# Performance work log

Hardware: AMD Instinct MI355X
Metric: run time of the kernel (lower is better)

Reference implementation:

```python
import jax, jax.numpy as jnp
import numpy as np

N, D_IN, D_OUT = 8192, 1024, 1024

def setup_inputs() -> dict:
    key = jax.random.key(0)
    k1, k2, k3, k4 = jax.random.split(key, 4)
    scale = 1.0 / np.sqrt(D_IN).astype(np.float32)
    return {
        "X": jax.random.normal(k1, (N, D_IN), dtype=jnp.float32),
        "W_Q": jax.random.normal(k2, (D_IN, D_OUT), dtype=jnp.float32) * scale,
        "W_K": jax.random.normal(k3, (D_IN, D_OUT), dtype=jnp.float32) * scale,
        "W_V": jax.random.normal(k4, (D_IN, D_OUT), dtype=jnp.float32) * scale,
    }

def reference(X, W_Q, W_K, W_V):
    # Manual single-head self-attention over the N rows of X.
    Q = X @ W_Q            # [N, d_out]
    Kmat = X @ W_K         # [N, d_out]
    V = X @ W_V            # [N, d_out]
    inv_sqrt_d = jnp.asarray(1.0 / np.sqrt(W_Q.shape[1]), dtype=Q.dtype)
    scores = (Q @ Kmat.T) * inv_sqrt_d            # [N, N]
    attn = jax.nn.softmax(scores, axis=-1)        # row-wise softmax (Keras default axis=-1)
    return attn @ V                               # [N, d_out]
```

## Files before the change

kernel.cpp:

```cpp
#include <hip/hip_runtime.h>

#define N_ROWS 8192
#define D_DIM  1024
#define SM_SHIFT 4.0f

typedef _Float16 f16;
typedef _Float16 f16x8 __attribute__((ext_vector_type(8)));
typedef _Float16 f16x4 __attribute__((ext_vector_type(4)));
typedef float    f32x4 __attribute__((ext_vector_type(4)));

__device__ __forceinline__ void gload16(const void* g, void* l) {
  __builtin_amdgcn_global_load_lds(
      (const __attribute__((address_space(1))) void*)g,
      (__attribute__((address_space(3))) void*)l, 16, 0, 0);
}

__device__ __forceinline__ int xcd_swz(int bid, int nb) {
  return (bid & 7) * (nb >> 3) + (bid >> 3);
}

__device__ __forceinline__ void tile2d4(int bid, int ny_t, int& nx, int& ny) {
  const int v = xcd_swz(bid, 32 * ny_t);
  const int g = v >> 4, w = v & 15;
  const int gpc = ny_t >> 2;
  const int gx = g / gpc, gy = g - gx * gpc;
  nx = gx * 4 + (w & 3);
  ny = gy * 4 + (w >> 2);
}

__global__ __launch_bounds__(256) void f32_to_f16_kernel(
    const float* __restrict__ in, f16* __restrict__ out, int n4) {
  for (int i = blockIdx.x * blockDim.x + threadIdx.x; i < n4;
       i += gridDim.x * blockDim.x) {
    float4 x = ((const float4*)in)[i];
    f16x4 h = {(f16)x.x, (f16)x.y, (f16)x.z, (f16)x.w};
    ((f16x4*)out)[i] = h;
  }
}

__global__ __launch_bounds__(256) void transpose_w_kernel(
    const float* __restrict__ w0, const float* __restrict__ w1,
    const float* __restrict__ w2, f16* __restrict__ WT) {
  const float* W = (blockIdx.z == 0) ? w0 : (blockIdx.z == 1) ? w1 : w2;
  f16* T = WT + (size_t)blockIdx.z * D_DIM * D_DIM;
  __shared__ float tile[64][65];
  const int r0 = blockIdx.y * 64, c0 = blockIdx.x * 64;
  const int t = threadIdx.x;
#pragma unroll
  for (int rep = 0; rep < 16; ++rep) {
    int idx = rep * 256 + t;
    int r = idx >> 6, c = idx & 63;
    tile[r][c] = W[(size_t)(r0 + r) * D_DIM + (c0 + c)];
  }
  __syncthreads();
#pragma unroll
  for (int rep = 0; rep < 16; ++rep) {
    int idx = rep * 256 + t;
    int r = idx >> 6, c = idx & 63;
    T[(size_t)(c0 + r) * D_DIM + (r0 + c)] = (f16)tile[c][r];
  }
}

template <bool SWAP>
__device__ __forceinline__ void mainloop256(const f16* __restrict__ Ag, int lda,
                                            const f16* __restrict__ Bg,
                                            int ldbt, int nk, f16* LA, f16* LB,
                                            f32x4 (&acc)[8][4], int tid) {
  const int lane = tid & 63;
  const int wr = tid >> 8, wc = (tid >> 6) & 3;
  const int ro = lane & 15;
  const int jj0 = (((lane >> 4) ^ (ro & 7)) << 4);
  const int rs = tid >> 3;
  const int ce = ((tid & 7) ^ (rs & 7)) * 8;
  const f16* a[4];
  const f16* b[4];
#pragma unroll
  for (int s = 0; s < 4; ++s) {
    a[s] = Ag + (size_t)(rs + 64 * s) * lda + ce;
    b[s] = Bg + (size_t)(rs + 64 * s) * ldbt + ce;
  }
  char* la = (char*)LA;
  char* lb = (char*)LB;
  const int t16 = tid * 16;

  auto stage_p0 = [&](int buf) {
    char* A = la + buf * 32768;
    char* B = lb + buf * 32768;
    gload16(a[0], A + t16);
    gload16(a[2], A + 16384 + t16);
    gload16(b[0], B + t16);
    gload16(b[1], B + 8192 + t16);
  };
  auto stage_p1 = [&](int buf) {
    char* A = la + buf * 32768;
    char* B = lb + buf * 32768;
    gload16(b[2], B + 16384 + t16);
    gload16(b[3], B + 24576 + t16);
    gload16(a[1], A + 8192 + t16);
    gload16(a[3], A + 24576 + t16);
#pragma unroll
    for (int s = 0; s < 4; ++s) {
      a[s] += 64;
      b[s] += 64;
    }
  };

  f16x8 af[4], bf[4];
  auto readA = [&](const char* ab, int h, int jo) {
#pragma unroll
    for (int j = 0; j < 4; ++j)
      af[j] = *(const f16x8*)(ab + (wr * 128 + h * 64 + j * 16 + ro) * 128 + jo);
  };
  auto readB = [&](const char* bb, int jo) {
#pragma unroll
    for (int ni = 0; ni < 4; ++ni)
      bf[ni] = *(const f16x8*)(bb + (wc * 64 + ni * 16 + ro) * 128 + jo);
  };

#define MFMA_CLUSTER(H)                                                   \
  asm volatile("s_waitcnt lgkmcnt(0)" ::: "memory");                      \
  __builtin_amdgcn_sched_barrier(0);                                      \
  __builtin_amdgcn_s_setprio(1);                                          \
  _Pragma("unroll") for (int j = 0; j < 4; ++j)                           \
  _Pragma("unroll") for (int ni = 0; ni < 4; ++ni)                        \
      acc[(H) * 4 + j][ni] =                                              \
          SWAP ? __builtin_amdgcn_mfma_f32_16x16x32_f16(bf[ni], af[j],    \
                                                        acc[(H) * 4 + j][ni], \
                                                        0, 0, 0)          \
               : __builtin_amdgcn_mfma_f32_16x16x32_f16(af[j], bf[ni],    \
                                                        acc[(H) * 4 + j][ni], \
                                                        0, 0, 0);         \
  __builtin_amdgcn_s_setprio(0);

  stage_p0(0);
  stage_p1(0);
  asm volatile("s_waitcnt vmcnt(0)" ::: "memory");
  __builtin_amdgcn_s_barrier();
  __builtin_amdgcn_sched_barrier(0);

  for (int kt = 0; kt < nk; ++kt) {
    const int buf = kt & 1;
    const char* ab = la + buf * 32768;
    const char* bb = lb + buf * 32768;
    const bool more = (kt + 1 < nk);
    readA(ab, 0, jj0);
    readB(bb, jj0);
    if (more) {
      stage_p0(buf ^ 1);
      asm volatile("s_waitcnt vmcnt(4)" ::: "memory");
    } else {
      asm volatile("s_waitcnt vmcnt(0)" ::: "memory");
    }
    __builtin_amdgcn_s_barrier();
    __builtin_amdgcn_sched_barrier(0);
    MFMA_CLUSTER(0)
    readA(ab, 1, jj0);
    if (more) stage_p1(buf ^ 1);
    MFMA_CLUSTER(1)
    readA(ab, 0, jj0 ^ 64);
    readB(bb, jj0 ^ 64);
    MFMA_CLUSTER(0)
    readA(ab, 1, jj0 ^ 64);
    MFMA_CLUSTER(1)
    asm volatile("s_waitcnt vmcnt(2)" ::: "memory");
    __builtin_amdgcn_s_barrier();
    __builtin_amdgcn_sched_barrier(0);
  }
#undef MFMA_CLUSTER
}

#define ACC_INIT8(acc)                                \
  _Pragma("unroll") for (int i = 0; i < 8; ++i)       \
      _Pragma("unroll") for (int j = 0; j < 4; ++j)   \
          acc[i][j] = (f32x4){0.f, 0.f, 0.f, 0.f};

__global__ __launch_bounds__(512, 2) void gemm_qkv(
    const f16* __restrict__ Xh, const f16* __restrict__ WT,
    f16* __restrict__ Q, f16* __restrict__ Kh, f16* __restrict__ VT) {
  __shared__ f16 LA[2][16384], LB[2][16384];
  const int v = xcd_swz(blockIdx.x, 384);
  const int z = v >> 7, r = v & 127;
  const int nx = r & 3, ny = r >> 2;
  const int tid = threadIdx.x, lane = tid & 63;
  const int wr = tid >> 8, wc = (tid >> 6) & 3;
  const int ro = lane & 15, rq = (lane >> 4) * 4;

  const f16* A = Xh + (size_t)ny * 256 * D_DIM;
  const f16* B = WT + (size_t)z * D_DIM * D_DIM + (size_t)nx * 256 * D_DIM;

  f32x4 acc[8][4];
  ACC_INIT8(acc);
  if (z < 2) {
    mainloop256<true>(A, D_DIM, B, D_DIM, D_DIM / 64, &LA[0][0], &LB[0][0],
                      acc, tid);
    f16* C = z ? Kh : Q;
#pragma unroll
    for (int mi = 0; mi < 8; ++mi) {
      const size_t xr = ny * 256 + wr * 128 + mi * 16 + ro;
#pragma unroll
      for (int ni = 0; ni < 4; ++ni) {
        f16x4 pk;
#pragma unroll
        for (int rr = 0; rr < 4; ++rr) pk[rr] = (f16)acc[mi][ni][rr];
        *(f16x4*)&C[xr * D_DIM + nx * 256 + wc * 64 + ni * 16 + rq] = pk;
      }
    }
  } else {
    mainloop256<false>(A, D_DIM, B, D_DIM, D_DIM / 64, &LA[0][0], &LB[0][0],
                       acc, tid);
#pragma unroll
    for (int mi = 0; mi < 8; ++mi)
#pragma unroll
      for (int ni = 0; ni < 4; ++ni) {
        f16x4 pk;
#pragma unroll
        for (int rr = 0; rr < 4; ++rr) pk[rr] = (f16)acc[mi][ni][rr];
        const size_t d = nx * 256 + wc * 64 + ni * 16 + ro;
        *(f16x4*)&VT[d * N_ROWS + ny * 256 + wr * 128 + mi * 16 + rq] = pk;
      }
  }
}

__global__ __launch_bounds__(512, 2) void gemm_s_exp(
    const f16* __restrict__ Q, const f16* __restrict__ Kh, f16* __restrict__ S,
    float* __restrict__ Lpart, int nyb) {
  __shared__ f16 LA[2][16384], LB[2][16384];
  int nx, ny;
  tile2d4(blockIdx.x, nyb, nx, ny);
  const int tid = threadIdx.x, lane = tid & 63;
  const int wr = tid >> 8, wc = (tid >> 6) & 3;
  const int ro = lane & 15, rq = (lane >> 4) * 4;

  f32x4 acc[8][4];
  ACC_INIT8(acc);
  mainloop256<true>(Q + (size_t)ny * 256 * D_DIM, D_DIM,
                    Kh + (size_t)nx * 256 * D_DIM, D_DIM, D_DIM / 64,
                    &LA[0][0], &LB[0][0], acc, tid);

  const float sc = 0.03125f;
#pragma unroll
  for (int mi = 0; mi < 8; ++mi) {
    const size_t q = ny * 256 + wr * 128 + mi * 16 + ro;
    f16* srow = S + q * N_ROWS + nx * 256 + wc * 64 + rq;
    float rs = 0.f;
#pragma unroll
    for (int ni = 0; ni < 4; ++ni) {
      f16x4 pk;
#pragma unroll
      for (int rr = 0; rr < 4; ++rr) {
        const float p = __expf(acc[mi][ni][rr] * sc - SM_SHIFT);
        rs += p;
        pk[rr] = (f16)p;
      }
      *(f16x4*)&srow[ni * 16] = pk;
    }
    rs += __shfl_xor(rs, 16, 64);
    rs += __shfl_xor(rs, 32, 64);
    if (lane < 16) Lpart[q * 128 + nx * 4 + wc] = rs;
  }
}

__global__ __launch_bounds__(256) void reduce_l(const float* __restrict__ Lpart,
                                                float* __restrict__ linv,
                                                int rows) {
  const int w = (blockIdx.x * 256 + threadIdx.x) >> 6;
  const int lane = threadIdx.x & 63;
  if (w >= rows) return;
  const float* p = Lpart + (size_t)w * 128;
  float s = p[lane] + p[lane + 64];
#pragma unroll
  for (int o = 32; o > 0; o >>= 1) s += __shfl_xor(s, o, 64);
  if (lane == 0) linv[w] = 1.0f / s;
}

__global__ __launch_bounds__(512, 2) void gemm_pv(const f16* __restrict__ S,
                                                  const f16* __restrict__ VT,
                                                  float* __restrict__ Ppart,
                                                  int nyb, int KS, int chunk) {
  __shared__ f16 LA[2][16384], LB[2][16384];
  const int nid = xcd_swz(blockIdx.x, (int)gridDim.x);
  const int nx = nid & 3, ny = (nid >> 2) % nyb, z = (nid >> 2) / nyb;
  const int tid = threadIdx.x, lane = tid & 63;
  const int wr = tid >> 8, wc = (tid >> 6) & 3;
  const int ro = lane & 15, rq = (lane >> 4) * 4;

  f32x4 acc[8][4];
  ACC_INIT8(acc);
  mainloop256<true>(S + (size_t)ny * 256 * N_ROWS + (size_t)z * KS, N_ROWS,
                    VT + (size_t)nx * 256 * N_ROWS + (size_t)z * KS, N_ROWS,
                    KS / 64, &LA[0][0], &LB[0][0], acc, tid);

  float* out = Ppart + (size_t)z * chunk * D_DIM;
#pragma unroll
  for (int mi = 0; mi < 8; ++mi) {
    const size_t q = ny * 256 + wr * 128 + mi * 16 + ro;
#pragma unroll
    for (int ni = 0; ni < 4; ++ni)
      *(f32x4*)&out[q * D_DIM + nx * 256 + wc * 64 + ni * 16 + rq] =
          acc[mi][ni];
  }
}

__global__ __launch_bounds__(256) void reduce_o(
    const float* __restrict__ Ppart, const float* __restrict__ linv,
    float* __restrict__ O, int rows, int sk) {
  const int n4 = rows * 256;
  const int stride = gridDim.x * blockDim.x;
  for (int i = blockIdx.x * 256 + threadIdx.x; i < n4; i += stride) {
    f32x4 s = ((const f32x4*)Ppart)[i];
    for (int t = 1; t < sk; ++t) s += ((const f32x4*)Ppart)[(size_t)t * n4 + i];
    const float il = linv[i >> 8];
    ((f32x4*)O)[i] = s * il;
  }
}

extern "C" void kernel_launch(void* const* d_in, const int* in_sizes, int n_in,
                              void* d_out, int out_size, void* d_ws,
                              size_t ws_size, hipStream_t stream) {
  (void)in_sizes;
  (void)n_in;
  (void)out_size;
  const float* X = (const float*)d_in[0];
  const float* WQ = (const float*)d_in[1];
  const float* WK = (const float*)d_in[2];
  const float* WV = (const float*)d_in[3];
  float* O = (float*)d_out;

  const size_t fixedA = (size_t)N_ROWS * D_DIM * 2 + 3ull * D_DIM * D_DIM * 2;
  int chunk = 1024, sk = 1;
  const int pref[][2] = {{8192, 2}, {4096, 2}, {2048, 2}, {8192, 1},
                         {4096, 1}, {2048, 1}, {1024, 1}};
  for (int i = 0; i < 7; ++i) {
    const int c = pref[i][0], s = pref[i][1];
    size_t R = (size_t)s * c * D_DIM * 4;
    if (R < fixedA) R = fixedA;
    const size_t need = R + 3ull * N_ROWS * D_DIM * 2 + (size_t)c * N_ROWS * 2 +
                        (size_t)c * 128 * 4 + (size_t)c * 4 + 4096;
    if (need <= ws_size) {
      chunk = c;
      sk = s;
      break;
    }
  }

  char* base = (char*)d_ws;
  f16* Xh = (f16*)base;
  f16* WT = (f16*)(base + (size_t)N_ROWS * D_DIM * 2);
  float* Ppart = (float*)base;
  size_t R = (size_t)sk * chunk * D_DIM * 4;
  if (R < fixedA) R = fixedA;
  char* p = base + ((R + 255) & ~(size_t)255);
  f16* Q = (f16*)p;
  p += (size_t)N_ROWS * D_DIM * 2;
  f16* Kh = (f16*)p;
  p += (size_t)N_ROWS * D_DIM * 2;
  f16* VT = (f16*)p;
  p += (size_t)N_ROWS * D_DIM * 2;
  f16* S = (f16*)p;
  p += (size_t)chunk * N_ROWS * 2;
  float* Lpart = (float*)p;
  p += (size_t)chunk * 128 * 4;
  float* linv = (float*)p;

  f32_to_f16_kernel<<<2048, 256, 0, stream>>>(X, Xh, N_ROWS * D_DIM / 4);
  transpose_w_kernel<<<dim3(16, 16, 3), 256, 0, stream>>>(WQ, WK, WV, WT);
  gemm_qkv<<<384, 512, 0, stream>>>(Xh, WT, Q, Kh, VT);

  const int KS = N_ROWS / sk;
  for (int mc = 0; mc < N_ROWS; mc += chunk) {
    const int nyb = chunk / 256;
    gemm_s_exp<<<32 * nyb, 512, 0, stream>>>(Q + (size_t)mc * D_DIM, Kh, S,
                                             Lpart, nyb);
    reduce_l<<<(chunk + 3) / 4, 256, 0, stream>>>(Lpart, linv, chunk);
    gemm_pv<<<4 * nyb * sk, 512, 0, stream>>>(S, VT, Ppart, nyb, KS, chunk);
    reduce_o<<<1024, 256, 0, stream>>>(Ppart, linv, O + (size_t)mc * D_DIM,
                                       chunk, sk);
  }
}
```

Baseline: 374.5 us.

## Merge split global-to-LDS staging into one phase and drop mid-loop barrier

The GEMM main loop used to issue the next K-tile's async global-to-LDS loads in two halves, with a partial vmcnt wait and an extra workgroup barrier in the middle of each iteration. Now all eight loads are issued together right after the first fragment reads, and the loop waits only once, with vmcnt(0) and a barrier at the end. The goal is to cut a barrier and a wait per iteration, leaving MFMA clusters less interrupted. In exchange, loads are less interleaved with compute, and the full drain at the end may expose more memory latency.

Result: slower. 382.9 us (+2.2%).

```diff
diff --git a/kernel.cpp b/kernel.cpp
--- a/kernel.cpp
+++ b/kernel.cpp
@@ -83,21 +83,14 @@
   char* lb = (char*)LB;
   const int t16 = tid * 16;
 
-  auto stage_p0 = [&](int buf) {
+  auto stage_all = [&](int buf) {
     char* A = la + buf * 32768;
     char* B = lb + buf * 32768;
-    gload16(a[0], A + t16);
-    gload16(a[2], A + 16384 + t16);
-    gload16(b[0], B + t16);
-    gload16(b[1], B + 8192 + t16);
-  };
-  auto stage_p1 = [&](int buf) {
-    char* A = la + buf * 32768;
-    char* B = lb + buf * 32768;
-    gload16(b[2], B + 16384 + t16);
-    gload16(b[3], B + 24576 + t16);
-    gload16(a[1], A + 8192 + t16);
-    gload16(a[3], A + 24576 + t16);
+#pragma unroll
+    for (int s = 0; s < 4; ++s) {
+      gload16(a[s], A + s * 8192 + t16);
+      gload16(b[s], B + s * 8192 + t16);
+    }
 #pragma unroll
     for (int s = 0; s < 4; ++s) {
       a[s] += 64;
@@ -132,8 +125,7 @@
                                                         0, 0, 0);         \
   __builtin_amdgcn_s_setprio(0);
 
-  stage_p0(0);
-  stage_p1(0);
+  stage_all(0);
   asm volatile("s_waitcnt vmcnt(0)" ::: "memory");
   __builtin_amdgcn_s_barrier();
   __builtin_amdgcn_sched_barrier(0);
@@ -142,27 +134,18 @@
     const int buf = kt & 1;
     const char* ab = la + buf * 32768;
     const char* bb = lb + buf * 32768;
-    const bool more = (kt + 1 < nk);
+    readB(bb, jj0);
     readA(ab, 0, jj0);
-    readB(bb, jj0);
-    if (more) {
-      stage_p0(buf ^ 1);
-      asm volatile("s_waitcnt vmcnt(4)" ::: "memory");
-    } else {
-      asm volatile("s_waitcnt vmcnt(0)" ::: "memory");
-    }
-    __builtin_amdgcn_s_barrier();
-    __builtin_amdgcn_sched_barrier(0);
+    if (kt + 1 < nk) stage_all(buf ^ 1);
     MFMA_CLUSTER(0)
     readA(ab, 1, jj0);
-    if (more) stage_p1(buf ^ 1);
     MFMA_CLUSTER(1)
+    readB(bb, jj0 ^ 64);
     readA(ab, 0, jj0 ^ 64);
-    readB(bb, jj0 ^ 64);
     MFMA_CLUSTER(0)
     readA(ab, 1, jj0 ^ 64);
     MFMA_CLUSTER(1)
-    asm volatile("s_waitcnt vmcnt(2)" ::: "memory");
+    asm volatile("s_waitcnt vmcnt(0)" ::: "memory");
     __builtin_amdgcn_s_barrier();
     __builtin_amdgcn_sched_barrier(0);
   }
```
